# Kernel tuning notes

Measured on AMD Instinct MI355X. Metric: run time of the kernel, lower is better.

## Reference

```python
import jax, jax.numpy as jnp
import numpy as np

B, S, DIM_IN, DIM_K, DIM_V = 4, 2048, 512, 2048, 64


def setup_inputs() -> dict:
    key = jax.random.key(0)
    k1, k2, k3, k4 = jax.random.split(key, 4)
    x = jax.random.normal(k1, (B, S, DIM_IN), dtype=jnp.float32)
    # nn.Linear(dim_in, d, bias=False) -> stored transposed here so y = x @ W
    Wq = jax.random.normal(k2, (DIM_IN, DIM_K), dtype=jnp.float32) / np.sqrt(DIM_IN)
    Wk = jax.random.normal(k3, (DIM_IN, DIM_K), dtype=jnp.float32) / np.sqrt(DIM_IN)
    Wv = jax.random.normal(k4, (DIM_IN, DIM_V), dtype=jnp.float32) / np.sqrt(DIM_IN)
    return {"x": x, "Wq": Wq, "Wk": Wk, "Wv": Wv}


def reference(x, Wq, Wk, Wv):
    dim_k = Wq.shape[-1]
    q = x @ Wq            # [B, S, dim_k]
    k = x @ Wk            # [B, S, dim_k]
    v = x @ Wv            # [B, S, dim_v]
    scores = jnp.einsum("bqd,bkd->bqk", q, k)  # [B, S, S]
    # causal mask: disallow attending to strictly-future positions
    seq = scores.shape[-1]
    mask = jnp.triu(jnp.ones((seq, seq), dtype=bool), k=1)
    scores = jnp.where(mask[None, :, :], -jnp.inf, scores)
    attn = jax.nn.softmax(scores / np.sqrt(dim_k).astype(np.float32), axis=-1)
    return attn @ v       # [B, S, dim_v]
```

## Files before the change

kernel.cpp:

```cpp
#include <hip/hip_runtime.h>
#include <hip/hip_bf16.h>

using bf16 = __hip_bfloat16;
typedef __bf16 bf16x8 __attribute__((ext_vector_type(8)));
typedef float floatx4 __attribute__((ext_vector_type(4)));

constexpr int BB = 4, SS = 2048, DIN = 512, DKK = 2048, DVV = 64;
constexpr int ROWS = BB * SS;
constexpr int LDY = 640;

constexpr size_t XB_OFF  = 0;
constexpr size_t WQB_OFF = XB_OFF  + 8388608;
constexpr size_t WKB_OFF = WQB_OFF + 2097152;
constexpr size_t WT2_OFF = WKB_OFF + 2097152;
constexpr size_t MTP_OFF = WT2_OFF + 655360;
constexpr size_t YV_OFF  = MTP_OFF + 8388608;
constexpr size_t VT_OFF  = YV_OFF  + 10485760;
constexpr size_t PRT_OFF = VT_OFF  + 1048576;
constexpr size_t STA_OFF = PRT_OFF + 16777216;

__device__ __forceinline__ void async_copy16(const bf16* g, const unsigned short* l) {
    __builtin_amdgcn_global_load_lds((const __attribute__((address_space(1))) void*)g,
                                     (__attribute__((address_space(3))) void*)l, 16, 0, 0);
}

__global__ __launch_bounds__(256) void prep(const float* __restrict__ x,
                                            const float* __restrict__ Wq,
                                            const float* __restrict__ Wk,
                                            const float* __restrict__ Wv,
                                            bf16* __restrict__ xb,
                                            bf16* __restrict__ wqb,
                                            bf16* __restrict__ wkb,
                                            bf16* __restrict__ wt2) {
    __shared__ float tile[32][33];
    const int bid = blockIdx.x;
    const int tid = threadIdx.x;

    if (bid < 4096) {
        int i = bid * 256 + tid;
        float4 v = reinterpret_cast<const float4*>(x)[i];
        union { bf16 h[4]; ushort4 u; } cv;
        cv.h[0] = __float2bfloat16(v.x);
        cv.h[1] = __float2bfloat16(v.y);
        cv.h[2] = __float2bfloat16(v.z);
        cv.h[3] = __float2bfloat16(v.w);
        reinterpret_cast<ushort4*>(xb)[i] = cv.u;
    } else if (bid < 6144) {
        int i = (bid - 4096) * 256 + tid;
        const float* src = (i < 262144) ? Wq : Wk;
        bf16* dst = (i < 262144) ? wqb : wkb;
        int j = (i < 262144) ? i : i - 262144;
        float4 v = reinterpret_cast<const float4*>(src)[j];
        union { bf16 h[4]; ushort4 u; } cv;
        cv.h[0] = __float2bfloat16(v.x);
        cv.h[1] = __float2bfloat16(v.y);
        cv.h[2] = __float2bfloat16(v.z);
        cv.h[3] = __float2bfloat16(v.w);
        reinterpret_cast<ushort4*>(dst)[j] = cv.u;
    } else {
        int idx = bid - 6144;
        int n0 = (idx & 1) * 32;
        int k0 = (idx >> 1) * 32;
        int nn = tid & 31, kk8 = tid >> 5;
        #pragma unroll
        for (int p = 0; p < 4; ++p) {
            int k = p * 8 + kk8;
            tile[k][nn] = Wv[(long long)(k0 + k) * 64 + n0 + nn];
        }
        __syncthreads();
        int kk = tid & 31, nn8 = tid >> 5;
        #pragma unroll
        for (int p = 0; p < 4; ++p) {
            int n = p * 8 + nn8;
            wt2[(long long)(512 + n0 + n) * 512 + k0 + kk] = __float2bfloat16(tile[kk][n]);
        }
    }
}

__global__ __launch_bounds__(256) void gemm_mt(const bf16* __restrict__ A,
                                               const bf16* __restrict__ Bt,
                                               float* __restrict__ Cp) {
    __shared__ __align__(16) unsigned short As[128 * 64];
    __shared__ __align__(16) unsigned short Bs[128 * 64];

    const int tid = threadIdx.x;
    const int lane = tid & 63, wave = tid >> 6;
    const long long m0 = (long long)blockIdx.y * 128;
    const long long n0 = (long long)blockIdx.x * 128;
    const int koff = blockIdx.z * 256;

    const int rIn = lane >> 3;
    const int cSwz = ((lane & 7) ^ rIn) * 8;
    const int wm0 = (wave >> 1) * 64, wn0 = (wave & 1) * 64;
    const int l15 = lane & 15, quad = lane >> 4;
    const int sw7 = l15 & 7;

    floatx4 acc[4][4] = {};

    for (int k0 = koff; k0 < koff + 256; k0 += 64) {
        #pragma unroll
        for (int t0 = 0; t0 < 8; ++t0) {
            int t = t0 * 4 + wave;
            if (t < 16)
                async_copy16(A + (m0 + t * 8 + rIn) * 2048LL + k0 + cSwz, &As[t * 512]);
            else
                async_copy16(Bt + (n0 + (t - 16) * 8 + rIn) * 2048LL + k0 + cSwz, &Bs[(t - 16) * 512]);
        }
        __syncthreads();
        #pragma unroll
        for (int sk = 0; sk < 2; ++sk) {
            const int rchunk = (((sk << 2) | quad) ^ sw7) * 8;
            bf16x8 af[4], bfr[4];
            #pragma unroll
            for (int mi = 0; mi < 4; ++mi)
                af[mi] = *reinterpret_cast<const bf16x8*>(&As[(wm0 + mi * 16 + l15) * 64 + rchunk]);
            #pragma unroll
            for (int ni = 0; ni < 4; ++ni)
                bfr[ni] = *reinterpret_cast<const bf16x8*>(&Bs[(wn0 + ni * 16 + l15) * 64 + rchunk]);
            #pragma unroll
            for (int mi = 0; mi < 4; ++mi)
                #pragma unroll
                for (int ni = 0; ni < 4; ++ni)
                    acc[mi][ni] = __builtin_amdgcn_mfma_f32_16x16x32_bf16(af[mi], bfr[ni],
                                                                          acc[mi][ni], 0, 0, 0);
        }
        __syncthreads();
    }

    float* C = Cp + (long long)blockIdx.z * 262144;
    #pragma unroll
    for (int mi = 0; mi < 4; ++mi) {
        long long row0 = m0 + wm0 + mi * 16 + quad * 4;
        #pragma unroll
        for (int ni = 0; ni < 4; ++ni) {
            long long col = n0 + wn0 + ni * 16 + l15;
            #pragma unroll
            for (int r = 0; r < 4; ++r)
                C[(row0 + r) * 512 + col] = acc[mi][ni][r];
        }
    }
}

__global__ __launch_bounds__(256) void reduce_mt(const float4* __restrict__ part,
                                                 bf16* __restrict__ wt2) {
    int i = blockIdx.x * 256 + threadIdx.x;
    float4 s = {0.f, 0.f, 0.f, 0.f};
    #pragma unroll
    for (int t = 0; t < 8; ++t) {
        float4 a = part[(long long)t * 65536 + i];
        s.x += a.x; s.y += a.y; s.z += a.z; s.w += a.w;
    }
    union { bf16 h[4]; ushort4 u; } cv;
    cv.h[0] = __float2bfloat16(s.x);
    cv.h[1] = __float2bfloat16(s.y);
    cv.h[2] = __float2bfloat16(s.z);
    cv.h[3] = __float2bfloat16(s.w);
    reinterpret_cast<ushort4*>(wt2)[i] = cv.u;
}

__global__ __launch_bounds__(256) void gemm_proj(const bf16* __restrict__ A,
                                                 const bf16* __restrict__ Bt,
                                                 bf16* __restrict__ C,
                                                 bf16* __restrict__ vt) {
    __shared__ __align__(16) unsigned short As[128 * 64];
    __shared__ __align__(16) unsigned short Bs[128 * 64];

    const int tid = threadIdx.x;
    const int lane = tid & 63, wave = tid >> 6;
    const long long m0 = (long long)blockIdx.y * 128;
    const long long n0 = (long long)blockIdx.x * 128;

    const int rIn = lane >> 3;
    const int cSwz = ((lane & 7) ^ rIn) * 8;
    const int wm0 = (wave >> 1) * 64, wn0 = (wave & 1) * 64;
    const int l15 = lane & 15, quad = lane >> 4;
    const int sw7 = l15 & 7;

    floatx4 acc[4][4] = {};

    for (int k0 = 0; k0 < DIN; k0 += 64) {
        #pragma unroll
        for (int t0 = 0; t0 < 8; ++t0) {
            int t = t0 * 4 + wave;
            if (t < 16)
                async_copy16(A + (m0 + t * 8 + rIn) * (long long)DIN + k0 + cSwz, &As[t * 512]);
            else
                async_copy16(Bt + (n0 + (t - 16) * 8 + rIn) * (long long)DIN + k0 + cSwz, &Bs[(t - 16) * 512]);
        }
        __syncthreads();
        #pragma unroll
        for (int sk = 0; sk < 2; ++sk) {
            const int rchunk = (((sk << 2) | quad) ^ sw7) * 8;
            bf16x8 af[4], bfr[4];
            #pragma unroll
            for (int mi = 0; mi < 4; ++mi)
                af[mi] = *reinterpret_cast<const bf16x8*>(&As[(wm0 + mi * 16 + l15) * 64 + rchunk]);
            #pragma unroll
            for (int ni = 0; ni < 4; ++ni)
                bfr[ni] = *reinterpret_cast<const bf16x8*>(&Bs[(wn0 + ni * 16 + l15) * 64 + rchunk]);
            #pragma unroll
            for (int mi = 0; mi < 4; ++mi)
                #pragma unroll
                for (int ni = 0; ni < 4; ++ni)
                    acc[mi][ni] = __builtin_amdgcn_mfma_f32_16x16x32_bf16(af[mi], bfr[ni],
                                                                          acc[mi][ni], 0, 0, 0);
        }
        __syncthreads();
    }

    if (n0 < 512) {
        #pragma unroll
        for (int mi = 0; mi < 4; ++mi) {
            long long row0 = m0 + wm0 + mi * 16 + quad * 4;
            #pragma unroll
            for (int ni = 0; ni < 4; ++ni) {
                long long col = n0 + wn0 + ni * 16 + l15;
                #pragma unroll
                for (int r = 0; r < 4; ++r)
                    C[(row0 + r) * (long long)LDY + col] = __float2bfloat16(acc[mi][ni][r]);
            }
        }
    } else if (!(wave & 1)) {
        const int b = (int)(m0 >> 11);
        const int sbase = ((int)m0 & 2047) + wm0;
        #pragma unroll
        for (int mi = 0; mi < 4; ++mi) {
            int s0 = sbase + mi * 16 + quad * 4;
            #pragma unroll
            for (int ni = 0; ni < 4; ++ni) {
                int j = ni * 16 + l15;
                union { bf16 h[4]; ushort4 u; } cv;
                #pragma unroll
                for (int r = 0; r < 4; ++r)
                    cv.h[r] = __float2bfloat16(acc[mi][ni][r]);
                *reinterpret_cast<ushort4*>(vt + ((long long)(b * DVV + j)) * SS + s0) = cv.u;
            }
        }
    }
}

__global__ __launch_bounds__(512) void attn_fused(const bf16* __restrict__ yv,
                                                  const bf16* __restrict__ xb,
                                                  const bf16* __restrict__ vt,
                                                  bf16* __restrict__ part,
                                                  float* __restrict__ stats) {
    constexpr int BK = 64;
    constexpr float SCALE = 0.022097086912079608f;

    __shared__ __align__(16) char smem[65536];
    unsigned short* As = (unsigned short*)smem;
    unsigned short* Bs = (unsigned short*)(smem + 32768);
    unsigned short* Ps = (unsigned short*)smem;
    unsigned short* Vs = (unsigned short*)(smem + 34816);
    float* smax = (float*)(smem + 52224);
    float* ssum = (float*)(smem + 53248);

    int T2 = (int)gridDim.y * 2;
    int xx = blockIdx.x, rr = blockIdx.y;
    int bx, by;
    if (xx <= rr) { by = rr; bx = xx; }
    else          { by = T2 - 1 - rr; bx = xx - rr - 1; }
    const int b = blockIdx.z;

    const bf16* A  = yv + (long long)b * SS * LDY;
    const bf16* Bt = xb + (long long)b * SS * 512;

    const int tid = threadIdx.x;
    const int lane = tid & 63, wave = tid >> 6;
    const long long m0 = (long long)by * 128;
    const long long n0 = (long long)bx * 128;

    const int rIn = lane >> 3;
    const int cSwz = ((lane & 7) ^ rIn) * 8;
    const int wm0 = (wave >> 1) * 32, wn0 = (wave & 1) * 64;
    const int l15 = lane & 15, quad = lane >> 4;
    const int sw7 = l15 & 7;

    floatx4 acc[2][4] = {};

    auto issue = [&](int buf, int k0) {
        #pragma unroll
        for (int t0 = 0; t0 < 4; ++t0) {
            int t = t0 * 8 + wave;
            if (t < 16)
                async_copy16(A + (m0 + t * 8 + rIn) * (long long)LDY + k0 + cSwz,
                             &As[buf * 8192 + t * 512]);
            else
                async_copy16(Bt + (n0 + (t - 16) * 8 + rIn) * 512LL + k0 + cSwz,
                             &Bs[buf * 8192 + (t - 16) * 512]);
        }
    };

    issue(0, 0);
    __syncthreads();
    for (int it = 0; it < DIN / BK; ++it) {
        const int cur = it & 1;
        if (it + 1 < DIN / BK) issue(cur ^ 1, (it + 1) * BK);
        #pragma unroll
        for (int sk = 0; sk < 2; ++sk) {
            const int rchunk = ((sk << 2) | quad) ^ sw7;
            bf16x8 af[2], bfr[4];
            #pragma unroll
            for (int mi = 0; mi < 2; ++mi)
                af[mi] = *reinterpret_cast<const bf16x8*>(
                    &As[cur * 8192 + (wm0 + mi * 16 + l15) * BK + rchunk * 8]);
            #pragma unroll
            for (int ni = 0; ni < 4; ++ni)
                bfr[ni] = *reinterpret_cast<const bf16x8*>(
                    &Bs[cur * 8192 + (wn0 + ni * 16 + l15) * BK + rchunk * 8]);
            #pragma unroll
            for (int mi = 0; mi < 2; ++mi)
                #pragma unroll
                for (int ni = 0; ni < 4; ++ni)
                    acc[mi][ni] = __builtin_amdgcn_mfma_f32_16x16x32_bf16(af[mi], bfr[ni],
                                                                          acc[mi][ni], 0, 0, 0);
        }
        __syncthreads();
    }

    #pragma unroll
    for (int mi = 0; mi < 2; ++mi)
        #pragma unroll
        for (int ni = 0; ni < 4; ++ni)
            #pragma unroll
            for (int r = 0; r < 4; ++r) {
                float v = acc[mi][ni][r] * SCALE;
                if (bx == by) {
                    int row = wm0 + mi * 16 + quad * 4 + r;
                    int col = wn0 + ni * 16 + l15;
                    if (col > row) v = -INFINITY;
                }
                acc[mi][ni][r] = v;
            }

    float rmax[2][4];
    #pragma unroll
    for (int mi = 0; mi < 2; ++mi)
        #pragma unroll
        for (int r = 0; r < 4; ++r) {
            float m = fmaxf(fmaxf(acc[mi][0][r], acc[mi][1][r]),
                            fmaxf(acc[mi][2][r], acc[mi][3][r]));
            #pragma unroll
            for (int msk = 8; msk >= 1; msk >>= 1) m = fmaxf(m, __shfl_xor(m, msk));
            rmax[mi][r] = m;
            if (l15 == 0) smax[(wm0 + mi * 16 + quad * 4 + r) * 2 + (wave & 1)] = m;
        }
    __syncthreads();
    #pragma unroll
    for (int mi = 0; mi < 2; ++mi)
        #pragma unroll
        for (int r = 0; r < 4; ++r) {
            int row = wm0 + mi * 16 + quad * 4 + r;
            rmax[mi][r] = fmaxf(smax[row * 2], smax[row * 2 + 1]);
        }

    #pragma unroll
    for (int mi = 0; mi < 2; ++mi)
        #pragma unroll
        for (int r = 0; r < 4; ++r) {
            float s = 0.f;
            #pragma unroll
            for (int ni = 0; ni < 4; ++ni) {
                float p = __expf(acc[mi][ni][r] - rmax[mi][r]);
                acc[mi][ni][r] = p;
                s += p;
            }
            #pragma unroll
            for (int msk = 8; msk >= 1; msk >>= 1) s += __shfl_xor(s, msk);
            if (l15 == 0) ssum[(wm0 + mi * 16 + quad * 4 + r) * 2 + (wave & 1)] = s;
        }
    #pragma unroll
    for (int mi = 0; mi < 2; ++mi) {
        int row = wm0 + mi * 16 + quad * 4;
        #pragma unroll
        for (int ni = 0; ni < 4; ++ni) {
            int col = wn0 + ni * 16 + l15;
            #pragma unroll
            for (int r = 0; r < 4; ++r)
                Ps[(row + r) * 136 + col] = (unsigned short)__bfloat16_as_ushort(__float2bfloat16(acc[mi][ni][r]));
        }
    }

    #pragma unroll
    for (int p = 0; p < 2; ++p) {
        int j = (tid >> 4) + p * 32;
        int ch = tid & 15;
        uint4 v = *reinterpret_cast<const uint4*>(
            vt + ((long long)b * DVV + j) * SS + n0 + ch * 8);
        *reinterpret_cast<uint4*>(&Vs[j * 136 + ((ch ^ (j & 7)) * 8)]) = v;
    }
    __syncthreads();

    if (tid < 128) {
        float m = fmaxf(smax[tid * 2], smax[tid * 2 + 1]);
        float l = ssum[tid * 2] + ssum[tid * 2 + 1];
        long long o = (((long long)b * 16 + bx) * SS + m0 + tid) * 2;
        stats[o] = m;
        stats[o + 1] = l;
    }

    const int wmv = wave * 16;
    floatx4 accO[4] = {};
    #pragma unroll
    for (int sk = 0; sk < 4; ++sk) {
        bf16x8 af = *reinterpret_cast<const bf16x8*>(
            &Ps[(wmv + l15) * 136 + sk * 32 + quad * 8]);
        #pragma unroll
        for (int ni = 0; ni < 4; ++ni) {
            bf16x8 bfv = *reinterpret_cast<const bf16x8*>(
                &Vs[(ni * 16 + l15) * 136 + ((((sk << 2) | quad)) ^ sw7) * 8]);
            accO[ni] = __builtin_amdgcn_mfma_f32_16x16x32_bf16(af, bfv, accO[ni], 0, 0, 0);
        }
    }
    #pragma unroll
    for (int ni = 0; ni < 4; ++ni)
        #pragma unroll
        for (int r = 0; r < 4; ++r)
            part[(((long long)b * 16 + bx) * SS + m0 + wmv + quad * 4 + r) * 64 + ni * 16 + l15]
                = __float2bfloat16(accO[ni][r]);
}

__global__ __launch_bounds__(256) void combine(const bf16* __restrict__ part,
                                               const float* __restrict__ stats,
                                               float* __restrict__ out) {
    int tid = blockIdx.x * 256 + threadIdx.x;
    int row = tid >> 3;
    int col8 = (tid & 7) * 8;
    int b = row >> 11, s = row & (SS - 1);
    int nt = (s >> 7) + 1;

    float m[16], l[16], M = -INFINITY;
    #pragma unroll
    for (int t = 0; t < 16; ++t)
        if (t < nt) {
            long long o = (((long long)b * 16 + t) * SS + s) * 2;
            m[t] = stats[o];
            l[t] = stats[o + 1];
            M = fmaxf(M, m[t]);
        }
    float O[8] = {};
    float L = 0.f;
    #pragma unroll
    for (int t = 0; t < 16; ++t)
        if (t < nt) {
            float wgt = __expf(m[t] - M);
            L += wgt * l[t];
            union { uint4 q; unsigned short u[8]; } ld;
            ld.q = *reinterpret_cast<const uint4*>(
                part + (((long long)b * 16 + t) * SS + s) * 64 + col8);
            #pragma unroll
            for (int j = 0; j < 8; ++j)
                O[j] += wgt * __uint_as_float((unsigned)ld.u[j] << 16);
        }
    float rinv = 1.0f / L;
    float4 o0 = {O[0] * rinv, O[1] * rinv, O[2] * rinv, O[3] * rinv};
    float4 o1 = {O[4] * rinv, O[5] * rinv, O[6] * rinv, O[7] * rinv};
    float4* dst = reinterpret_cast<float4*>(out + (long long)row * 64 + col8);
    dst[0] = o0;
    dst[1] = o1;
}

extern "C" void kernel_launch(void* const* d_in, const int* in_sizes, int n_in,
                              void* d_out, int out_size, void* d_ws, size_t ws_size,
                              hipStream_t stream) {
    const float* x  = (const float*)d_in[0];
    const float* Wq = (const float*)d_in[1];
    const float* Wk = (const float*)d_in[2];
    const float* Wv = (const float*)d_in[3];
    float* out = (float*)d_out;

    char* w = (char*)d_ws;
    bf16* xb   = (bf16*)(w + XB_OFF);
    bf16* wqb  = (bf16*)(w + WQB_OFF);
    bf16* wkb  = (bf16*)(w + WKB_OFF);
    bf16* wt2  = (bf16*)(w + WT2_OFF);
    float* mtp = (float*)(w + MTP_OFF);
    bf16* yv   = (bf16*)(w + YV_OFF);
    bf16* vt   = (bf16*)(w + VT_OFF);
    bf16* part = (bf16*)(w + PRT_OFF);
    float* stats = (float*)(w + STA_OFF);

    prep<<<6176, 256, 0, stream>>>(x, Wq, Wk, Wv, xb, wqb, wkb, wt2);

    gemm_mt<<<dim3(4, 4, 8), 256, 0, stream>>>(wkb, wqb, mtp);
    reduce_mt<<<65536 / 256, 256, 0, stream>>>((const float4*)mtp, wt2);

    gemm_proj<<<dim3(LDY / 128, ROWS / 128, 1), 256, 0, stream>>>(xb, wt2, yv, vt);

    attn_fused<<<dim3(SS / 128 + 1, SS / 256, BB), 512, 0, stream>>>(yv, xb, vt, part, stats);

    combine<<<ROWS * 8 / 256, 256, 0, stream>>>(part, stats, out);
}
```

Measured before the change: 146.9 us.

## Remap workgroup IDs for XCD-local L2 reuse and prefetch V early

Flattens the grids of the three GEMM/attention kernels and remaps the block index with an XCD-aware permutation (blockIdx & 7 chooses the chiplet), so tiles that share A or B rows run on the same XCD and reuse its L2. The causal attention kernel now decodes a triangular tile index through a sqrt-based inverse instead of the old folded-rectangle mapping. It also loads the V tile into registers at kernel start so that global load overlaps the QK GEMM. The cost is extra register pressure and some index arithmetic, and the new tile order changes how causal work is balanced across blocks.

```diff
diff --git a/kernel.cpp b/kernel.cpp
--- a/kernel.cpp
+++ b/kernel.cpp
@@ -1,5 +1,6 @@
 #include <hip/hip_runtime.h>
 #include <hip/hip_bf16.h>
+#include <math.h>
 
 using bf16 = __hip_bfloat16;
 typedef __bf16 bf16x8 __attribute__((ext_vector_type(8)));
@@ -85,9 +86,13 @@
 
     const int tid = threadIdx.x;
     const int lane = tid & 63, wave = tid >> 6;
-    const long long m0 = (long long)blockIdx.y * 128;
-    const long long n0 = (long long)blockIdx.x * 128;
-    const int koff = blockIdx.z * 256;
+
+    const int wg = (blockIdx.x & 7) * 16 + (blockIdx.x >> 3);
+    const int z = wg >> 4;
+    const int tile = wg & 15;
+    const long long m0 = (long long)(tile >> 2) * 128;
+    const long long n0 = (long long)(tile & 3) * 128;
+    const int koff = z * 256;
 
     const int rIn = lane >> 3;
     const int cSwz = ((lane & 7) ^ rIn) * 8;
@@ -127,7 +132,7 @@
         __syncthreads();
     }
 
-    float* C = Cp + (long long)blockIdx.z * 262144;
+    float* C = Cp + (long long)z * 262144;
     #pragma unroll
     for (int mi = 0; mi < 4; ++mi) {
         long long row0 = m0 + wm0 + mi * 16 + quad * 4;
@@ -167,8 +172,10 @@
 
     const int tid = threadIdx.x;
     const int lane = tid & 63, wave = tid >> 6;
-    const long long m0 = (long long)blockIdx.y * 128;
-    const long long n0 = (long long)blockIdx.x * 128;
+
+    const int wg = (blockIdx.x & 7) * 40 + (blockIdx.x >> 3);
+    const long long m0 = (long long)(wg / 5) * 128;
+    const long long n0 = (long long)(wg % 5) * 128;
 
     const int rIn = lane >> 3;
     const int cSwz = ((lane & 7) ^ rIn) * 8;
@@ -255,11 +262,11 @@
     float* smax = (float*)(smem + 52224);
     float* ssum = (float*)(smem + 53248);
 
-    int T2 = (int)gridDim.y * 2;
-    int xx = blockIdx.x, rr = blockIdx.y;
-    int bx, by;
-    if (xx <= rr) { by = rr; bx = xx; }
-    else          { by = T2 - 1 - rr; bx = xx - rr - 1; }
+    const int wg = (blockIdx.x & 7) * 17 + (blockIdx.x >> 3);
+    int by = (int)((sqrtf(8.f * (float)wg + 1.f) - 1.f) * 0.5f);
+    while ((by + 1) * (by + 2) / 2 <= wg) ++by;
+    while (by * (by + 1) / 2 > wg) --by;
+    const int bx = wg - by * (by + 1) / 2;
     const int b = blockIdx.z;
 
     const bf16* A  = yv + (long long)b * SS * LDY;
@@ -277,6 +284,15 @@
     const int sw7 = l15 & 7;
 
     floatx4 acc[2][4] = {};
+
+    uint4 vreg[2];
+    #pragma unroll
+    for (int p = 0; p < 2; ++p) {
+        int j = (tid >> 4) + p * 32;
+        int ch = tid & 15;
+        vreg[p] = *reinterpret_cast<const uint4*>(
+            vt + ((long long)b * DVV + j) * SS + n0 + ch * 8);
+    }
 
     auto issue = [&](int buf, int k0) {
         #pragma unroll
@@ -385,9 +401,7 @@
     for (int p = 0; p < 2; ++p) {
         int j = (tid >> 4) + p * 32;
         int ch = tid & 15;
-        uint4 v = *reinterpret_cast<const uint4*>(
-            vt + ((long long)b * DVV + j) * SS + n0 + ch * 8);
-        *reinterpret_cast<uint4*>(&Vs[j * 136 + ((ch ^ (j & 7)) * 8)]) = v;
+        *reinterpret_cast<uint4*>(&Vs[j * 136 + ((ch ^ (j & 7)) * 8)]) = vreg[p];
     }
     __syncthreads();
 
@@ -482,12 +496,12 @@
 
     prep<<<6176, 256, 0, stream>>>(x, Wq, Wk, Wv, xb, wqb, wkb, wt2);
 
-    gemm_mt<<<dim3(4, 4, 8), 256, 0, stream>>>(wkb, wqb, mtp);
+    gemm_mt<<<128, 256, 0, stream>>>(wkb, wqb, mtp);
     reduce_mt<<<65536 / 256, 256, 0, stream>>>((const float4*)mtp, wt2);
 
-    gemm_proj<<<dim3(LDY / 128, ROWS / 128, 1), 256, 0, stream>>>(xb, wt2, yv, vt);
-
-    attn_fused<<<dim3(SS / 128 + 1, SS / 256, BB), 512, 0, stream>>>(yv, xb, vt, part, stats);
+    gemm_proj<<<320, 256, 0, stream>>>(xb, wt2, yv, vt);
+
+    attn_fused<<<dim3(136, 1, BB), 512, 0, stream>>>(yv, xb, vt, part, stats);
 
     combine<<<ROWS * 8 / 256, 256, 0, stream>>>(part, stats, out);
 }
```

Result: no change. 144.2 us (-1.8%).
